# Kernel optimization log

Measured on AMD Instinct MI355X. Metric: run time of the kernel, lower is better.

The kernel has to match this reference:

```python
import jax, jax.numpy as jnp
import numpy as np

B, T, C, HS = 8, 2048, 2048, 128  # batch, seq, n_embedding, head_size
THETA = 10000.0


def _rope_tables(dim, seq_len, theta=THETA):
    freqs = 1.0 / theta ** (jnp.arange(0, dim, 2, dtype=jnp.float32) / dim)  # [dim/2]
    t = jnp.arange(seq_len, dtype=jnp.float32)
    ang = jnp.outer(t, freqs)  # [T, dim/2]
    return jnp.cos(ang), jnp.sin(ang)


def _apply_rope(v, cos, sin):
    # v: [B,T,D]; pairs along last dim treated as complex (real=even, imag=odd)
    b, t, d = v.shape
    vr = v.reshape(b, t, d // 2, 2)
    x0, x1 = vr[..., 0], vr[..., 1]
    o0 = x0 * cos - x1 * sin
    o1 = x0 * sin + x1 * cos
    return jnp.stack([o0, o1], axis=-1).reshape(b, t, d)


def setup_inputs() -> dict:
    key = jax.random.key(0)
    k1, k2, k3, k4 = jax.random.split(key, 4)
    scale = 1.0 / np.sqrt(C)
    x = jax.random.normal(k1, (B, T, C), dtype=jnp.float32)
    Wk = jax.random.normal(k2, (C, HS), dtype=jnp.float32) * scale
    Wq = jax.random.normal(k3, (C, HS), dtype=jnp.float32) * scale
    Wv = jax.random.normal(k4, (C, HS), dtype=jnp.float32) * scale
    return {"x": x, "Wk": Wk, "Wq": Wq, "Wv": Wv}


def reference(x, Wk, Wq, Wv):
    b, t, _ = x.shape
    cos, sin = _rope_tables(HS, t)
    k = x @ Wk  # [B,T,HS]
    q = x @ Wq
    # Source: xq,xk = apply_rotary_emb(key, query); query,key = xq,xk
    # => scores = rope(q_proj) @ rope(k_proj)^T (standard causal attention)
    qr = _apply_rope(q, cos, sin)
    kr = _apply_rope(k, cos, sin)
    scores = jnp.einsum('btd,bsd->bts', qr, kr) * (HS ** -0.5)  # [B,T,T]
    causal = jnp.tril(jnp.ones((t, t), dtype=bool))
    scores = jnp.where(causal, scores, -jnp.inf)
    wei = jax.nn.softmax(scores, axis=-1)
    v = x @ Wv
    return jnp.einsum('bts,bsd->btd', wei, v)
```

## Files before the change

kernel.cpp:

```cpp
#include <hip/hip_runtime.h>

#define NB 8
#define NT 2048
#define NC 2048
#define NH 128

typedef short s8v __attribute__((ext_vector_type(8)));
typedef float f4  __attribute__((ext_vector_type(4)));

static __device__ __forceinline__ unsigned short f2bf(float f) {
    union { float f; unsigned int u; } v; v.f = f;
    unsigned int x = v.u;
    return (unsigned short)((x + 0x7FFFu + ((x >> 16) & 1u)) >> 16);
}

static __device__ __forceinline__ void gl2lds16(const void* g, void* lds_base) {
    __builtin_amdgcn_global_load_lds(
        (const __attribute__((address_space(1))) unsigned int*)g,
        (__attribute__((address_space(3))) unsigned int*)lds_base, 16, 0, 0);
}

__global__ __launch_bounds__(256) void wtrans_k(
    const float* __restrict__ Wk, const float* __restrict__ Wq,
    const float* __restrict__ Wv, unsigned short* __restrict__ wt)
{
    __shared__ float Ls[64][129];
    const int mat = blockIdx.y;
    const float* W = (mat == 0) ? Wq : (mat == 1) ? Wk : Wv;
    const int k0 = blockIdx.x * 64;
    const int t  = threadIdx.x;

    #pragma unroll
    for (int j = 0; j < 8; ++j) {
        int flat = j * 1024 + t * 4;
        int k = flat >> 7, n = flat & 127;
        f4 v = *reinterpret_cast<const f4*>(W + (size_t)(k0 + k) * NH + n);
        Ls[k][n] = v[0]; Ls[k][n + 1] = v[1]; Ls[k][n + 2] = v[2]; Ls[k][n + 3] = v[3];
    }
    __syncthreads();

    const int n = t >> 1, half = t & 1;
    unsigned short tmp[32];
    #pragma unroll
    for (int kk = 0; kk < 32; ++kk) tmp[kk] = f2bf(Ls[half * 32 + kk][n]);
    unsigned short* dst = wt + (size_t)mat * 262144 + (size_t)n * 2048 + k0 + half * 32;
    #pragma unroll
    for (int v = 0; v < 4; ++v)
        *reinterpret_cast<s8v*>(dst + v * 8) = *reinterpret_cast<s8v*>(tmp + v * 8);
}

__global__ __launch_bounds__(256) void proj_rope(
    const float* __restrict__ x, const unsigned short* __restrict__ wt,
    unsigned short* __restrict__ qws, unsigned short* __restrict__ kws,
    unsigned short* __restrict__ vtws)
{
    __shared__ char LDS[49152];
    char* AsB = LDS;
    char* BsB = LDS + 16384;

    const int mat  = blockIdx.y;
    const int tid  = threadIdx.x;
    const int wave = tid >> 6;
    const int lane = tid & 63;
    const int quad = lane >> 4, l16 = lane & 15;
    const int wm = wave >> 1, wn = wave & 1;
    const int M0 = blockIdx.x * 64;
    const unsigned short* wtm = wt + mat * (NH * NC);

    const float* asrc[8];
    unsigned int adst[8];
    #pragma unroll
    for (int s = 0; s < 8; ++s) {
        const int f   = tid + s * 256;
        const int row = f >> 5;
        const int kc  = (f & 31) * 4;
        asrc[s] = x + (size_t)(M0 + row) * NC + kc;
        const int c   = kc >> 3;
        const int pos = c ^ (row & 15);
        adst[s] = row * 256 + pos * 16 + (kc & 4) * 2;
    }

    const unsigned short* bsrc[8];
    #pragma unroll
    for (int s = 0; s < 8; ++s) {
        const int j   = wave * 8 + s;
        const int row = j * 4 + (lane >> 4);
        const int c   = (lane & 15) ^ (row & 15);
        bsrc[s] = wtm + (size_t)row * NC + c * 8;
    }

    f4 acc[2][4];
    #pragma unroll
    for (int mi = 0; mi < 2; ++mi)
        #pragma unroll
        for (int ni = 0; ni < 4; ++ni)
            acc[mi][ni] = (f4){0.f, 0.f, 0.f, 0.f};

    for (int kk = 0; kk < NC; kk += 128) {
        #pragma unroll
        for (int s = 0; s < 8; ++s)
            gl2lds16(bsrc[s] + kk, BsB + (wave * 8 + s) * 1024);

        #pragma unroll
        for (int s = 0; s < 8; ++s) {
            union { f4 f; unsigned int u[4]; } v;
            v.f = *reinterpret_cast<const f4*>(asrc[s] + kk);
            unsigned int d0 = __builtin_amdgcn_perm(v.u[1], v.u[0], 0x07060302u);
            unsigned int d1 = __builtin_amdgcn_perm(v.u[3], v.u[2], 0x07060302u);
            uint2 p; p.x = d0; p.y = d1;
            *reinterpret_cast<uint2*>(AsB + adst[s]) = p;
        }
        __syncthreads();

        #pragma unroll
        for (int ksub = 0; ksub < 4; ++ksub) {
            const int c = ksub * 4 + quad;
            s8v a[2];
            #pragma unroll
            for (int mi = 0; mi < 2; ++mi) {
                const int row = wm * 32 + mi * 16 + l16;
                a[mi] = *reinterpret_cast<const s8v*>(AsB + row * 256 + (c ^ l16) * 16);
            }
            #pragma unroll
            for (int ni = 0; ni < 4; ++ni) {
                const int row2 = wn * 64 + ni * 16 + l16;
                s8v b = *reinterpret_cast<const s8v*>(BsB + row2 * 256 + (c ^ l16) * 16);
                acc[0][ni] = __builtin_amdgcn_mfma_f32_16x16x32_bf16(a[0], b, acc[0][ni], 0, 0, 0);
                acc[1][ni] = __builtin_amdgcn_mfma_f32_16x16x32_bf16(a[1], b, acc[1][ni], 0, 0, 0);
            }
        }
        __syncthreads();
    }

    const float cfreq = -0.10381025296f;
    #pragma unroll
    for (int mi = 0; mi < 2; ++mi) {
        #pragma unroll
        for (int ni = 0; ni < 4; ++ni) {
            const int col = wn * 64 + ni * 16 + l16;
            #pragma unroll
            for (int r = 0; r < 4; ++r) {
                const int row = M0 + wm * 32 + mi * 16 + quad * 4 + r;
                const int t   = row & (NT - 1);
                float v = acc[mi][ni][r];
                if (mat < 2) {
                    float other = __shfl_xor(v, 1, 64);
                    float freq  = exp2f(cfreq * (float)(col & ~1));
                    float ang   = (float)t * freq;
                    float sn = sinf(ang), cs = cosf(ang);
                    v = (col & 1) ? (other * sn + v * cs)
                                  : (v * cs - other * sn);
                }
                unsigned short bv = f2bf(v);
                if (mat == 0)      qws[(size_t)row * NH + col] = bv;
                else if (mat == 1) kws[(size_t)row * NH + col] = bv;
                else {
                    int b = row >> 11;
                    vtws[(size_t)b * (NH * NT) + (size_t)col * NT + t] = bv;
                }
            }
        }
    }
}

__global__ __launch_bounds__(256, 2) void attn_k(
    const unsigned short* __restrict__ qws, const unsigned short* __restrict__ kws,
    const unsigned short* __restrict__ vtws, float* __restrict__ out)
{
    __shared__ unsigned short P[4][32 * 64];
    __shared__ float Os[4][32][64];
    __shared__ float Ms[4][32], Ls[4][32], Lt[32];

    const int wave = threadIdx.x >> 6;
    const int lane = threadIdx.x & 63;
    const int quad = lane >> 4, l16 = lane & 15;
    const int b     = blockIdx.y;
    const int qrow0 = blockIdx.x * 32;
    const unsigned short* Q  = qws  + (size_t)b * NT * NH;
    const unsigned short* K  = kws  + (size_t)b * NT * NH;
    const unsigned short* Vt = vtws + (size_t)b * NH * NT;

    s8v qf[2][4];
    #pragma unroll
    for (int mi = 0; mi < 2; ++mi)
        #pragma unroll
        for (int ks = 0; ks < 4; ++ks)
            qf[mi][ks] = *reinterpret_cast<const s8v*>(
                Q + (size_t)(qrow0 + mi * 16 + l16) * NH + ks * 32 + quad * 8);

    float m[2][4], ls[2][4];
    f4 o[2][8];
    #pragma unroll
    for (int mi = 0; mi < 2; ++mi) {
        #pragma unroll
        for (int r = 0; r < 4; ++r) { m[mi][r] = -INFINITY; ls[mi][r] = 0.f; }
        #pragma unroll
        for (int dt = 0; dt < 8; ++dt) o[mi][dt] = (f4){0.f, 0.f, 0.f, 0.f};
    }

    const int nkt = (qrow0 >> 6) + 1;
    const float scale = 0.0883883476f;

    for (int kt = wave; kt < nkt; kt += 4) {
        const int kbase = kt * 64;
        const bool domask = (kt == nkt - 1);

        f4 s[2][4];
        #pragma unroll
        for (int nt = 0; nt < 4; ++nt) {
            f4 a0 = (f4){0.f, 0.f, 0.f, 0.f}, a1 = a0;
            #pragma unroll
            for (int ks = 0; ks < 4; ++ks) {
                s8v kf = *reinterpret_cast<const s8v*>(
                    K + (size_t)(kbase + nt * 16 + l16) * NH + ks * 32 + quad * 8);
                a0 = __builtin_amdgcn_mfma_f32_16x16x32_bf16(qf[0][ks], kf, a0, 0, 0, 0);
                a1 = __builtin_amdgcn_mfma_f32_16x16x32_bf16(qf[1][ks], kf, a1, 0, 0, 0);
            }
            s[0][nt] = a0; s[1][nt] = a1;
        }

        #pragma unroll
        for (int mi = 0; mi < 2; ++mi) {
            #pragma unroll
            for (int r = 0; r < 4; ++r) {
                const int trow = qrow0 + mi * 16 + quad * 4 + r;
                #pragma unroll
                for (int nt = 0; nt < 4; ++nt) {
                    float sv = s[mi][nt][r] * scale;
                    if (domask && (kbase + nt * 16 + l16 > trow)) sv = -INFINITY;
                    s[mi][nt][r] = sv;
                }
                float tm = fmaxf(fmaxf(s[mi][0][r], s[mi][1][r]),
                                 fmaxf(s[mi][2][r], s[mi][3][r]));
                #pragma unroll
                for (int off = 1; off < 16; off <<= 1)
                    tm = fmaxf(tm, __shfl_xor(tm, off, 64));
                const float mn = fmaxf(m[mi][r], tm);
                const float alpha = __expf(m[mi][r] - mn);
                m[mi][r] = mn;
                float rs = 0.f;
                #pragma unroll
                for (int nt = 0; nt < 4; ++nt) {
                    float p = __expf(s[mi][nt][r] - mn);
                    s[mi][nt][r] = p;
                    rs += p;
                }
                ls[mi][r] = ls[mi][r] * alpha + rs;
                #pragma unroll
                for (int dt = 0; dt < 8; ++dt) o[mi][dt][r] *= alpha;
            }
        }

        #pragma unroll
        for (int mi = 0; mi < 2; ++mi)
            #pragma unroll
            for (int nt = 0; nt < 4; ++nt)
                #pragma unroll
                for (int r = 0; r < 4; ++r) {
                    const int prow = mi * 16 + quad * 4 + r;
                    const int swz  = ((nt * 2 + (l16 >> 3)) ^ (prow & 7)) * 8 + (l16 & 7);
                    P[wave][prow * 64 + swz] = f2bf(s[mi][nt][r]);
                }

        #pragma unroll
        for (int ks2 = 0; ks2 < 2; ++ks2) {
            s8v pa[2];
            #pragma unroll
            for (int mi = 0; mi < 2; ++mi) {
                const int prow = mi * 16 + l16;
                const int pp = ((ks2 * 4 + quad) ^ (l16 & 7));
                pa[mi] = *reinterpret_cast<const s8v*>(&P[wave][prow * 64 + pp * 8]);
            }
            #pragma unroll
            for (int dt = 0; dt < 8; ++dt) {
                s8v vf = *reinterpret_cast<const s8v*>(
                    Vt + (size_t)(dt * 16 + l16) * NT + kbase + ks2 * 32 + quad * 8);
                o[0][dt] = __builtin_amdgcn_mfma_f32_16x16x32_bf16(pa[0], vf, o[0][dt], 0, 0, 0);
                o[1][dt] = __builtin_amdgcn_mfma_f32_16x16x32_bf16(pa[1], vf, o[1][dt], 0, 0, 0);
            }
        }
    }

    #pragma unroll
    for (int mi = 0; mi < 2; ++mi)
        #pragma unroll
        for (int r = 0; r < 4; ++r) {
            float v = ls[mi][r];
            #pragma unroll
            for (int off = 1; off < 16; off <<= 1) v += __shfl_xor(v, off, 64);
            ls[mi][r] = v;
        }

    if (l16 == 0) {
        #pragma unroll
        for (int mi = 0; mi < 2; ++mi)
            #pragma unroll
            for (int r = 0; r < 4; ++r) {
                Ms[wave][mi * 16 + quad * 4 + r] = m[mi][r];
                Ls[wave][mi * 16 + quad * 4 + r] = ls[mi][r];
            }
    }
    __syncthreads();

    #pragma unroll
    for (int mi = 0; mi < 2; ++mi)
        #pragma unroll
        for (int r = 0; r < 4; ++r) {
            const int row = mi * 16 + quad * 4 + r;
            float M = fmaxf(fmaxf(Ms[0][row], Ms[1][row]), fmaxf(Ms[2][row], Ms[3][row]));
            float sc = __expf(m[mi][r] - M);
            float lt = Ls[0][row] * __expf(Ms[0][row] - M) + Ls[1][row] * __expf(Ms[1][row] - M)
                     + Ls[2][row] * __expf(Ms[2][row] - M) + Ls[3][row] * __expf(Ms[3][row] - M);
            if (wave == 0 && l16 == 0) Lt[row] = lt;
            #pragma unroll
            for (int dt = 0; dt < 8; ++dt) o[mi][dt][r] *= sc;
        }

    const int rrow = threadIdx.x >> 3;
    const int cx   = (threadIdx.x & 7) * 8;
    #pragma unroll
    for (int h = 0; h < 2; ++h) {
        __syncthreads();
        #pragma unroll
        for (int mi = 0; mi < 2; ++mi)
            #pragma unroll
            for (int dtl = 0; dtl < 4; ++dtl)
                #pragma unroll
                for (int r = 0; r < 4; ++r)
                    Os[wave][mi * 16 + quad * 4 + r][dtl * 16 + l16] = o[mi][h * 4 + dtl][r];
        __syncthreads();
        f4 s0 = (f4){0.f, 0.f, 0.f, 0.f}, s1 = s0;
        #pragma unroll
        for (int w = 0; w < 4; ++w) {
            s0 += *reinterpret_cast<const f4*>(&Os[w][rrow][cx]);
            s1 += *reinterpret_cast<const f4*>(&Os[w][rrow][cx + 4]);
        }
        const float rl = 1.0f / Lt[rrow];
        float* dst = &out[((size_t)b * NT + qrow0 + rrow) * NH + h * 64 + cx];
        *reinterpret_cast<f4*>(dst)     = s0 * rl;
        *reinterpret_cast<f4*>(dst + 4) = s1 * rl;
    }
}

extern "C" void kernel_launch(void* const* d_in, const int* in_sizes, int n_in,
                              void* d_out, int out_size, void* d_ws, size_t ws_size,
                              hipStream_t stream) {
    const float* x  = (const float*)d_in[0];
    const float* Wk = (const float*)d_in[1];
    const float* Wq = (const float*)d_in[2];
    const float* Wv = (const float*)d_in[3];
    unsigned short* ws   = (unsigned short*)d_ws;
    unsigned short* wt   = ws;
    unsigned short* qws  = ws  + 786432;
    unsigned short* kws  = qws + 2097152;
    unsigned short* vtws = kws + 2097152;
    float* outp = (float*)d_out;

    wtrans_k<<<dim3(32, 3), 256, 0, stream>>>(Wk, Wq, Wv, wt);
    proj_rope<<<dim3(256, 3), 256, 0, stream>>>(x, wt, qws, kws, vtws);
    attn_k<<<dim3(64, 8), 256, 0, stream>>>(qws, kws, vtws, outp);
}
```

Baseline: 336.5 us.

## Halve attention query tile to 16 rows and prefetch projection A operand

The attention kernel now processes 16 query rows per block instead of 32, doubling the grid and raising launch bounds to 3 blocks per CU. The goal is more parallelism and better balance across the causal triangle, at the cost of reloading K/V tiles for half as many query rows each time. Separately, the projection kernel register-prefetches the next fp32 x chunk before the barrier so global load latency overlaps the MFMA work.

```diff
diff --git a/kernel.cpp b/kernel.cpp
--- a/kernel.cpp
+++ b/kernel.cpp
@@ -96,6 +96,11 @@
         for (int ni = 0; ni < 4; ++ni)
             acc[mi][ni] = (f4){0.f, 0.f, 0.f, 0.f};
 
+    f4 areg[8];
+    #pragma unroll
+    for (int s = 0; s < 8; ++s)
+        areg[s] = *reinterpret_cast<const f4*>(asrc[s]);
+
     for (int kk = 0; kk < NC; kk += 128) {
         #pragma unroll
         for (int s = 0; s < 8; ++s)
@@ -103,12 +108,16 @@
 
         #pragma unroll
         for (int s = 0; s < 8; ++s) {
-            union { f4 f; unsigned int u[4]; } v;
-            v.f = *reinterpret_cast<const f4*>(asrc[s] + kk);
-            unsigned int d0 = __builtin_amdgcn_perm(v.u[1], v.u[0], 0x07060302u);
-            unsigned int d1 = __builtin_amdgcn_perm(v.u[3], v.u[2], 0x07060302u);
-            uint2 p; p.x = d0; p.y = d1;
+            union { f4 f; unsigned int u[4]; } v; v.f = areg[s];
+            uint2 p;
+            p.x = __builtin_amdgcn_perm(v.u[1], v.u[0], 0x07060302u);
+            p.y = __builtin_amdgcn_perm(v.u[3], v.u[2], 0x07060302u);
             *reinterpret_cast<uint2*>(AsB + adst[s]) = p;
+        }
+        if (kk + 128 < NC) {
+            #pragma unroll
+            for (int s = 0; s < 8; ++s)
+                areg[s] = *reinterpret_cast<const f4*>(asrc[s] + kk + 128);
         }
         __syncthreads();
 
@@ -163,40 +172,35 @@
     }
 }
 
-__global__ __launch_bounds__(256, 2) void attn_k(
+__global__ __launch_bounds__(256, 3) void attn_k(
     const unsigned short* __restrict__ qws, const unsigned short* __restrict__ kws,
     const unsigned short* __restrict__ vtws, float* __restrict__ out)
 {
-    __shared__ unsigned short P[4][32 * 64];
-    __shared__ float Os[4][32][64];
-    __shared__ float Ms[4][32], Ls[4][32], Lt[32];
+    __shared__ unsigned short P[4][16 * 64];
+    __shared__ float Os[4][16][64];
+    __shared__ float Ms[4][16], Ls[4][16], Lt[16];
 
     const int wave = threadIdx.x >> 6;
     const int lane = threadIdx.x & 63;
     const int quad = lane >> 4, l16 = lane & 15;
     const int b     = blockIdx.y;
-    const int qrow0 = blockIdx.x * 32;
+    const int qrow0 = blockIdx.x * 16;
     const unsigned short* Q  = qws  + (size_t)b * NT * NH;
     const unsigned short* K  = kws  + (size_t)b * NT * NH;
     const unsigned short* Vt = vtws + (size_t)b * NH * NT;
 
-    s8v qf[2][4];
-    #pragma unroll
-    for (int mi = 0; mi < 2; ++mi)
-        #pragma unroll
-        for (int ks = 0; ks < 4; ++ks)
-            qf[mi][ks] = *reinterpret_cast<const s8v*>(
-                Q + (size_t)(qrow0 + mi * 16 + l16) * NH + ks * 32 + quad * 8);
-
-    float m[2][4], ls[2][4];
-    f4 o[2][8];
-    #pragma unroll
-    for (int mi = 0; mi < 2; ++mi) {
-        #pragma unroll
-        for (int r = 0; r < 4; ++r) { m[mi][r] = -INFINITY; ls[mi][r] = 0.f; }
-        #pragma unroll
-        for (int dt = 0; dt < 8; ++dt) o[mi][dt] = (f4){0.f, 0.f, 0.f, 0.f};
-    }
+    s8v qf[4];
+    #pragma unroll
+    for (int ks = 0; ks < 4; ++ks)
+        qf[ks] = *reinterpret_cast<const s8v*>(
+            Q + (size_t)(qrow0 + l16) * NH + ks * 32 + quad * 8);
+
+    float m[4], ls[4];
+    f4 o[8];
+    #pragma unroll
+    for (int r = 0; r < 4; ++r) { m[r] = -INFINITY; ls[r] = 0.f; }
+    #pragma unroll
+    for (int dt = 0; dt < 8; ++dt) o[dt] = (f4){0.f, 0.f, 0.f, 0.f};
 
     const int nkt = (qrow0 >> 6) + 1;
     const float scale = 0.0883883476f;
@@ -205,140 +209,116 @@
         const int kbase = kt * 64;
         const bool domask = (kt == nkt - 1);
 
-        f4 s[2][4];
+        f4 s[4];
         #pragma unroll
         for (int nt = 0; nt < 4; ++nt) {
-            f4 a0 = (f4){0.f, 0.f, 0.f, 0.f}, a1 = a0;
+            f4 a = (f4){0.f, 0.f, 0.f, 0.f};
             #pragma unroll
             for (int ks = 0; ks < 4; ++ks) {
                 s8v kf = *reinterpret_cast<const s8v*>(
                     K + (size_t)(kbase + nt * 16 + l16) * NH + ks * 32 + quad * 8);
-                a0 = __builtin_amdgcn_mfma_f32_16x16x32_bf16(qf[0][ks], kf, a0, 0, 0, 0);
-                a1 = __builtin_amdgcn_mfma_f32_16x16x32_bf16(qf[1][ks], kf, a1, 0, 0, 0);
-            }
-            s[0][nt] = a0; s[1][nt] = a1;
-        }
-
-        #pragma unroll
-        for (int mi = 0; mi < 2; ++mi) {
+                a = __builtin_amdgcn_mfma_f32_16x16x32_bf16(qf[ks], kf, a, 0, 0, 0);
+            }
+            s[nt] = a;
+        }
+
+        #pragma unroll
+        for (int r = 0; r < 4; ++r) {
+            const int trow = qrow0 + quad * 4 + r;
+            #pragma unroll
+            for (int nt = 0; nt < 4; ++nt) {
+                float sv = s[nt][r] * scale;
+                if (domask && (kbase + nt * 16 + l16 > trow)) sv = -INFINITY;
+                s[nt][r] = sv;
+            }
+            float tm = fmaxf(fmaxf(s[0][r], s[1][r]), fmaxf(s[2][r], s[3][r]));
+            #pragma unroll
+            for (int off = 1; off < 16; off <<= 1)
+                tm = fmaxf(tm, __shfl_xor(tm, off, 64));
+            const float mn = fmaxf(m[r], tm);
+            const float alpha = __expf(m[r] - mn);
+            m[r] = mn;
+            float rs = 0.f;
+            #pragma unroll
+            for (int nt = 0; nt < 4; ++nt) {
+                float p = __expf(s[nt][r] - mn);
+                s[nt][r] = p;
+                rs += p;
+            }
+            ls[r] = ls[r] * alpha + rs;
+            #pragma unroll
+            for (int dt = 0; dt < 8; ++dt) o[dt][r] *= alpha;
+        }
+
+        #pragma unroll
+        for (int nt = 0; nt < 4; ++nt)
             #pragma unroll
             for (int r = 0; r < 4; ++r) {
-                const int trow = qrow0 + mi * 16 + quad * 4 + r;
-                #pragma unroll
-                for (int nt = 0; nt < 4; ++nt) {
-                    float sv = s[mi][nt][r] * scale;
-                    if (domask && (kbase + nt * 16 + l16 > trow)) sv = -INFINITY;
-                    s[mi][nt][r] = sv;
-                }
-                float tm = fmaxf(fmaxf(s[mi][0][r], s[mi][1][r]),
-                                 fmaxf(s[mi][2][r], s[mi][3][r]));
-                #pragma unroll
-                for (int off = 1; off < 16; off <<= 1)
-                    tm = fmaxf(tm, __shfl_xor(tm, off, 64));
-                const float mn = fmaxf(m[mi][r], tm);
-                const float alpha = __expf(m[mi][r] - mn);
-                m[mi][r] = mn;
-                float rs = 0.f;
-                #pragma unroll
-                for (int nt = 0; nt < 4; ++nt) {
-                    float p = __expf(s[mi][nt][r] - mn);
-                    s[mi][nt][r] = p;
-                    rs += p;
-                }
-                ls[mi][r] = ls[mi][r] * alpha + rs;
-                #pragma unroll
-                for (int dt = 0; dt < 8; ++dt) o[mi][dt][r] *= alpha;
-            }
-        }
-
-        #pragma unroll
-        for (int mi = 0; mi < 2; ++mi)
-            #pragma unroll
-            for (int nt = 0; nt < 4; ++nt)
-                #pragma unroll
-                for (int r = 0; r < 4; ++r) {
-                    const int prow = mi * 16 + quad * 4 + r;
-                    const int swz  = ((nt * 2 + (l16 >> 3)) ^ (prow & 7)) * 8 + (l16 & 7);
-                    P[wave][prow * 64 + swz] = f2bf(s[mi][nt][r]);
-                }
+                const int prow = quad * 4 + r;
+                const int swz  = ((nt * 2 + (l16 >> 3)) ^ (prow & 7)) * 8 + (l16 & 7);
+                P[wave][prow * 64 + swz] = f2bf(s[nt][r]);
+            }
 
         #pragma unroll
         for (int ks2 = 0; ks2 < 2; ++ks2) {
-            s8v pa[2];
-            #pragma unroll
-            for (int mi = 0; mi < 2; ++mi) {
-                const int prow = mi * 16 + l16;
-                const int pp = ((ks2 * 4 + quad) ^ (l16 & 7));
-                pa[mi] = *reinterpret_cast<const s8v*>(&P[wave][prow * 64 + pp * 8]);
-            }
+            const int pp = (ks2 * 4 + quad) ^ (l16 & 7);
+            s8v pa = *reinterpret_cast<const s8v*>(&P[wave][l16 * 64 + pp * 8]);
             #pragma unroll
             for (int dt = 0; dt < 8; ++dt) {
                 s8v vf = *reinterpret_cast<const s8v*>(
                     Vt + (size_t)(dt * 16 + l16) * NT + kbase + ks2 * 32 + quad * 8);
-                o[0][dt] = __builtin_amdgcn_mfma_f32_16x16x32_bf16(pa[0], vf, o[0][dt], 0, 0, 0);
-                o[1][dt] = __builtin_amdgcn_mfma_f32_16x16x32_bf16(pa[1], vf, o[1][dt], 0, 0, 0);
-            }
-        }
-    }
-
-    #pragma unroll
-    for (int mi = 0; mi < 2; ++mi)
+                o[dt] = __builtin_amdgcn_mfma_f32_16x16x32_bf16(pa, vf, o[dt], 0, 0, 0);
+            }
+        }
+    }
+
+    #pragma unroll
+    for (int r = 0; r < 4; ++r) {
+        float v = ls[r];
+        #pragma unroll
+        for (int off = 1; off < 16; off <<= 1) v += __shfl_xor(v, off, 64);
+        ls[r] = v;
+    }
+
+    if (l16 == 0) {
         #pragma unroll
         for (int r = 0; r < 4; ++r) {
-            float v = ls[mi][r];
-            #pragma unroll
-            for (int off = 1; off < 16; off <<= 1) v += __shfl_xor(v, off, 64);
-            ls[mi][r] = v;
-        }
-
-    if (l16 == 0) {
-        #pragma unroll
-        for (int mi = 0; mi < 2; ++mi)
-            #pragma unroll
-            for (int r = 0; r < 4; ++r) {
-                Ms[wave][mi * 16 + quad * 4 + r] = m[mi][r];
-                Ls[wave][mi * 16 + quad * 4 + r] = ls[mi][r];
-            }
+            Ms[wave][quad * 4 + r] = m[r];
+            Ls[wave][quad * 4 + r] = ls[r];
+        }
     }
     __syncthreads();
 
     #pragma unroll
-    for (int mi = 0; mi < 2; ++mi)
-        #pragma unroll
-        for (int r = 0; r < 4; ++r) {
-            const int row = mi * 16 + quad * 4 + r;
-            float M = fmaxf(fmaxf(Ms[0][row], Ms[1][row]), fmaxf(Ms[2][row], Ms[3][row]));
-            float sc = __expf(m[mi][r] - M);
-            float lt = Ls[0][row] * __expf(Ms[0][row] - M) + Ls[1][row] * __expf(Ms[1][row] - M)
-                     + Ls[2][row] * __expf(Ms[2][row] - M) + Ls[3][row] * __expf(Ms[3][row] - M);
-            if (wave == 0 && l16 == 0) Lt[row] = lt;
-            #pragma unroll
-            for (int dt = 0; dt < 8; ++dt) o[mi][dt][r] *= sc;
-        }
-
-    const int rrow = threadIdx.x >> 3;
-    const int cx   = (threadIdx.x & 7) * 8;
+    for (int r = 0; r < 4; ++r) {
+        const int row = quad * 4 + r;
+        float M = fmaxf(fmaxf(Ms[0][row], Ms[1][row]), fmaxf(Ms[2][row], Ms[3][row]));
+        float sc = __expf(m[r] - M);
+        float lt = Ls[0][row] * __expf(Ms[0][row] - M) + Ls[1][row] * __expf(Ms[1][row] - M)
+                 + Ls[2][row] * __expf(Ms[2][row] - M) + Ls[3][row] * __expf(Ms[3][row] - M);
+        if (wave == 0 && l16 == 0) Lt[row] = lt;
+        #pragma unroll
+        for (int dt = 0; dt < 8; ++dt) o[dt][r] *= sc;
+    }
+
+    const int rrow = threadIdx.x >> 4;
+    const int cx   = (threadIdx.x & 15) * 4;
     #pragma unroll
     for (int h = 0; h < 2; ++h) {
         __syncthreads();
         #pragma unroll
-        for (int mi = 0; mi < 2; ++mi)
-            #pragma unroll
-            for (int dtl = 0; dtl < 4; ++dtl)
-                #pragma unroll
-                for (int r = 0; r < 4; ++r)
-                    Os[wave][mi * 16 + quad * 4 + r][dtl * 16 + l16] = o[mi][h * 4 + dtl][r];
+        for (int dtl = 0; dtl < 4; ++dtl)
+            #pragma unroll
+            for (int r = 0; r < 4; ++r)
+                Os[wave][quad * 4 + r][dtl * 16 + l16] = o[h * 4 + dtl][r];
         __syncthreads();
-        f4 s0 = (f4){0.f, 0.f, 0.f, 0.f}, s1 = s0;
-        #pragma unroll
-        for (int w = 0; w < 4; ++w) {
-            s0 += *reinterpret_cast<const f4*>(&Os[w][rrow][cx]);
-            s1 += *reinterpret_cast<const f4*>(&Os[w][rrow][cx + 4]);
-        }
+        f4 sum = (f4){0.f, 0.f, 0.f, 0.f};
+        #pragma unroll
+        for (int w = 0; w < 4; ++w)
+            sum += *reinterpret_cast<const f4*>(&Os[w][rrow][cx]);
         const float rl = 1.0f / Lt[rrow];
-        float* dst = &out[((size_t)b * NT + qrow0 + rrow) * NH + h * 64 + cx];
-        *reinterpret_cast<f4*>(dst)     = s0 * rl;
-        *reinterpret_cast<f4*>(dst + 4) = s1 * rl;
+        *reinterpret_cast<f4*>(
+            &out[((size_t)b * NT + qrow0 + rrow) * NH + h * 64 + cx]) = sum * rl;
     }
 }
 
@@ -358,5 +338,5 @@
 
     wtrans_k<<<dim3(32, 3), 256, 0, stream>>>(Wk, Wq, Wv, wt);
     proj_rope<<<dim3(256, 3), 256, 0, stream>>>(x, wt, qws, kws, vtws);
-    attn_k<<<dim3(64, 8), 256, 0, stream>>>(qws, kws, vtws, outp);
-}
+    attn_k<<<dim3(128, 8), 256, 0, stream>>>(qws, kws, vtws, outp);
+}
```

Result: no change. 342.7 us (+1.8%).
